# Performance work log

Measured on AMD Instinct MI355X. Metric: run time of the kernel, lower is better.

## Reference

```python
import jax, jax.numpy as jnp
import numpy as np

N_NODES = 100000
N_EDGES = 1200000
D = 64
EPS = 1e-12  # matches torch F.normalize eps


def l2norm(x):
    n = jnp.linalg.norm(x, axis=-1, keepdims=True)
    return x / jnp.maximum(n, EPS)


def sage_layer(x, src, dst, Wl, bl, Wr, scale):
    # mechanism.normalize: row-wise L2 normalize (noise_scale=0 -> perturb is identity)
    xn = l2norm(x)
    # agg = x_normalized + scatter-add of neighbor (source) features into targets
    agg = xn + jax.ops.segment_sum(xn[src], dst, num_segments=N_NODES)
    # MessageNorm(learn_scale=True): normalize(msg) * ||x||_2 * scale
    msg = l2norm(agg) * jnp.linalg.norm(x, axis=-1, keepdims=True) * scale
    # lin_l(msg) + lin_r(x)  (root_weight=True, lin_r has no bias)
    out = msg @ Wl.T + bl + x @ Wr.T
    return l2norm(out)


def setup_inputs() -> dict:
    key = jax.random.key(0)
    ks = jax.random.split(key, 7)
    s = 1.0 / np.sqrt(D)
    return {
        "x": jax.random.normal(ks[0], (N_NODES, D), jnp.float32),
        "Wl0": jax.random.normal(ks[1], (D, D), jnp.float32) * s,
        "bl0": jnp.zeros((D,), jnp.float32),
        "Wr0": jax.random.normal(ks[2], (D, D), jnp.float32) * s,
        "scale0": jnp.ones((), jnp.float32),
        "Wl1": jax.random.normal(ks[3], (D, D), jnp.float32) * s,
        "bl1": jnp.zeros((D,), jnp.float32),
        "Wr1": jax.random.normal(ks[4], (D, D), jnp.float32) * s,
        "scale1": jnp.ones((), jnp.float32),
        "edge_index": jax.random.randint(ks[5], (2, N_EDGES), 0, N_NODES, dtype=jnp.int32),
    }


def reference(x, Wl0, bl0, Wr0, scale0, Wl1, bl1, Wr1, scale1, edge_index):
    src, dst = edge_index[0], edge_index[1]
    h = sage_layer(x, src, dst, Wl0, bl0, Wr0, scale0)
    h = jax.nn.relu(h)  # activation after layer 0 (not pred layer); dropout=identity (eval)
    h = sage_layer(h, src, dst, Wl1, bl1, Wr1, scale1)
    return h  # last layer of pred module: no bn/dropout/activation
```

## Files before the change

kernel.cpp:

```cpp
#include <hip/hip_runtime.h>

#define D 64
#define EPS 1e-12f
#define WPITCH 68
#define BSHIFT 8
#define BW 256
#define NBMAX 2048
#define NBLK 256

typedef unsigned short u16;

__device__ __forceinline__ float bf2f(u16 u) {
    return __uint_as_float(((unsigned)u) << 16);
}
__device__ __forceinline__ u16 f2bf(float f) {
    unsigned u = __float_as_uint(f);
    u += 0x7fffu + ((u >> 16) & 1u);
    return (u16)(u >> 16);
}
__device__ __forceinline__ float loadf(const void* p, size_t i, int bf) {
    return bf ? bf2f(((const u16*)p)[i]) : ((const float*)p)[i];
}
__device__ __forceinline__ float4 cvt4(ushort4 u) {
    return make_float4(bf2f(u.x), bf2f(u.y), bf2f(u.z), bf2f(u.w));
}

#define FMA4(acc, s, v)                       \
    do {                                      \
        acc.x = fmaf((s), (v).x, acc.x);      \
        acc.y = fmaf((s), (v).y, acc.y);      \
        acc.z = fmaf((s), (v).z, acc.z);      \
        acc.w = fmaf((s), (v).w, acc.w);      \
    } while (0)

__global__ __launch_bounds__(64) void detect_kernel(const u16* __restrict__ x,
                                                    int* __restrict__ flag) {
    int lane = threadIdx.x;
    int bad = 0;
    for (int i = 0; i < 64; ++i) {
        u16 u = x[lane * 64 + i];
        int e = (u >> 7) & 0xFF;
        if (e >= 0xC0) bad = 1;
    }
    unsigned long long b = __ballot(bad);
    if (lane == 0) *flag = (b == 0ull) ? 1 : 0;
}


__global__ __launch_bounds__(256) void zero_kernel(int* __restrict__ a, int n) {
    int i = blockIdx.x * blockDim.x + threadIdx.x;
    if (i < n) a[i] = 0;
}

__global__ __launch_bounds__(256) void bhist_kernel(const int* __restrict__ dst,
                                                    int* __restrict__ blockhist,
                                                    int E, int NB) {
    __shared__ int lh[NBMAX];
    const int b = blockIdx.x, t = threadIdx.x;
    const int per = (E + NBLK - 1) / NBLK;
    const int e0 = b * per, e1 = min(E, e0 + per);
    if (NB <= NBMAX) {
        for (int i = t; i < NB; i += 256) lh[i] = 0;
        __syncthreads();
        for (int e = e0 + t; e < e1; e += 256)
            atomicAdd(&lh[dst[e] >> BSHIFT], 1);
        __syncthreads();
        for (int i = t; i < NB; i += 256) blockhist[i * NBLK + b] = lh[i];
    } else {
        for (int e = e0 + t; e < e1; e += 256)
            atomicAdd(&blockhist[(dst[e] >> BSHIFT) * NBLK + b], 1);
    }
}

__global__ __launch_bounds__(256) void scanA_kernel(const int* __restrict__ a,
                                                    int* __restrict__ partials, int M) {
    int b = blockIdx.x, t = threadIdx.x;
    int base = b * 1024 + t * 4;
    int s = 0;
#pragma unroll
    for (int i = 0; i < 4; ++i) {
        int idx = base + i;
        if (idx < M) s += a[idx];
    }
    s += __shfl_xor(s, 32); s += __shfl_xor(s, 16); s += __shfl_xor(s, 8);
    s += __shfl_xor(s, 4);  s += __shfl_xor(s, 2);  s += __shfl_xor(s, 1);
    __shared__ int wt[4];
    if ((t & 63) == 0) wt[t >> 6] = s;
    __syncthreads();
    if (t == 0) partials[b] = wt[0] + wt[1] + wt[2] + wt[3];
}

__global__ __launch_bounds__(64) void scanB_kernel(int* __restrict__ partials, int NP) {
    int l = threadIdx.x;
    int total = 0;
    for (int base = 0; base < NP; base += 64) {
        int v = (base + l < NP) ? partials[base + l] : 0;
        int inc = v;
        for (int d = 1; d < 64; d <<= 1) {
            int u = __shfl_up(inc, d);
            if (l >= d) inc += u;
        }
        if (base + l < NP) partials[base + l] = inc - v + total;
        total += __shfl(inc, 63);
    }
}

__global__ __launch_bounds__(256) void scanC_kernel(const int* __restrict__ a,
                                                    const int* __restrict__ partials,
                                                    int* __restrict__ pos, int M) {
    int b = blockIdx.x, t = threadIdx.x;
    int base = b * 1024 + t * 4;
    int v[4];
    int s = 0;
#pragma unroll
    for (int i = 0; i < 4; ++i) {
        int idx = base + i;
        v[i] = (idx < M) ? a[idx] : 0;
        s += v[i];
    }
    int li = t & 63, w = t >> 6;
    int inc = s;
    for (int d = 1; d < 64; d <<= 1) {
        int u = __shfl_up(inc, d);
        if (li >= d) inc += u;
    }
    __shared__ int wt[4];
    if (li == 63) wt[w] = inc;
    __syncthreads();
    int woff = 0;
    for (int i = 0; i < w; ++i) woff += wt[i];
    int run = partials[b] + woff + (inc - s);
#pragma unroll
    for (int i = 0; i < 4; ++i) {
        int idx = base + i;
        if (idx < M) { pos[idx] = run; run += v[i]; }
    }
}

__global__ __launch_bounds__(256) void bmeta_kernel(const int* __restrict__ pos,
                                                    int* __restrict__ bcounts,
                                                    int* __restrict__ boffsets,
                                                    int NB, int E) {
    int i = blockIdx.x * blockDim.x + threadIdx.x;
    if (i < NB) {
        int s = pos[(size_t)i * NBLK];
        boffsets[i] = s;
        int nxt = (i + 1 < NB) ? pos[(size_t)(i + 1) * NBLK] : E;
        bcounts[i] = nxt - s;
    }
}

__global__ __launch_bounds__(256) void bfill_kernel(const int* __restrict__ src,
                                                    const int* __restrict__ dst,
                                                    int* __restrict__ pos,
                                                    int* __restrict__ bucket,
                                                    int E, int NB) {
    __shared__ int cur[NBMAX];
    const int b = blockIdx.x, t = threadIdx.x;
    const int per = (E + NBLK - 1) / NBLK;
    const int e0 = b * per, e1 = min(E, e0 + per);
    if (NB <= NBMAX) {
        for (int i = t; i < NB; i += 256) cur[i] = pos[(size_t)i * NBLK + b];
        __syncthreads();
        for (int e = e0 + t; e < e1; e += 256) {
            int s = src[e], d = dst[e];
            int p = atomicAdd(&cur[d >> BSHIFT], 1);
            bucket[p] = (s << BSHIFT) | (d & (BW - 1));
        }
    } else {
        for (int e = e0 + t; e < e1; e += 256) {
            int s = src[e], d = dst[e];
            int p = atomicAdd(&pos[(size_t)(d >> BSHIFT) * NBLK + b], 1);
            bucket[p] = (s << BSHIFT) | (d & (BW - 1));
        }
    }
}

__global__ __launch_bounds__(256) void csr_from_buckets_kernel(
    const int* __restrict__ bucket,
    const int* __restrict__ bcounts, const int* __restrict__ boffsets,
    int* __restrict__ counts, int* __restrict__ offsets,
    int* __restrict__ sorted_src, int N)
{
    __shared__ int hist[BW];
    __shared__ int cur[BW];
    __shared__ int wt[4];

    const int b = blockIdx.x;
    const int t = threadIdx.x;
    const int nbase = b << BSHIFT;
    const int ecnt = bcounts[b];
    const int ebase = boffsets[b];

    hist[t] = 0;
    __syncthreads();

    for (int e = t; e < ecnt; e += 256)
        atomicAdd(&hist[bucket[ebase + e] & (BW - 1)], 1);
    __syncthreads();

    int v = hist[t];
    int inc = v;
    for (int d = 1; d < 64; d <<= 1) {
        int u = __shfl_up(inc, d);
        if ((t & 63) >= d) inc += u;
    }
    if ((t & 63) == 63) wt[t >> 6] = inc;
    __syncthreads();
    int woff = 0;
    for (int i = 0; i < (t >> 6); ++i) woff += wt[i];
    int excl = inc - v + woff;
    cur[t] = excl;
    int node = nbase + t;
    if (node < N) {
        counts[node] = v;
        offsets[node] = ebase + excl;
    }
    __syncthreads();

    for (int e = t; e < ecnt; e += 256) {
        int pv = bucket[ebase + e];
        int p = atomicAdd(&cur[pv & (BW - 1)], 1);
        sorted_src[ebase + p] = ((unsigned)pv) >> BSHIFT;
    }
}


__global__ __launch_bounds__(256) void norm_init_kernel(
    const void* __restrict__ xin, float* __restrict__ nx, float* __restrict__ rnx,
    int N, const int* __restrict__ flagp)
{
    const int bf = *flagp;
    int node = (int)((blockIdx.x * blockDim.x + threadIdx.x) >> 6);
    int lane = threadIdx.x & 63;
    if (node >= N) return;
    float v = loadf(xin, (size_t)node * D + lane, bf);
    float s = v * v;
    s += __shfl_xor(s, 32); s += __shfl_xor(s, 16); s += __shfl_xor(s, 8);
    s += __shfl_xor(s, 4);  s += __shfl_xor(s, 2);  s += __shfl_xor(s, 1);
    if (lane == 0) {
        float n = sqrtf(s);
        nx[node] = n;
        rnx[node] = 1.0f / fmaxf(n, EPS);
    }
}

__device__ __forceinline__ float4 loadrow4(const void* p, int row, int lane16, int bf) {
    if (bf) {
        ushort4 u = ((const ushort4*)((const u16*)p + (size_t)row * D))[lane16];
        return cvt4(u);
    }
    return ((const float4*)((const float*)p + (size_t)row * D))[lane16];
}

__global__ __launch_bounds__(256) void gather_kernel(
    const int* __restrict__ offsets, const int* __restrict__ counts,
    const int* __restrict__ sorted_src,
    const void* __restrict__ xin, const float* __restrict__ rnx,
    float* __restrict__ agg, int N, const int* __restrict__ flagp)
{
    const int bf = *flagp;
    int node = (int)((blockIdx.x * blockDim.x + threadIdx.x) >> 6);
    int lane = threadIdx.x & 63;
    if (node >= N) return;
    const int lane16 = lane & 15, grp = lane >> 4;

    float4 acc = make_float4(0.f, 0.f, 0.f, 0.f);
    if (grp == 0) {
        float4 xs = loadrow4(xin, node, lane16, bf);
        FMA4(acc, rnx[node], xs);
    }

    const int start = offsets[node];
    const int deg = counts[node];
    for (int i = 0; i < deg; i += 64) {
        int cnt = min(deg - i, 64);
        int id = (lane < cnt) ? sorted_src[start + i + lane] : 0;
        float wvl = rnx[id];
        int j = 0;
        for (; j + 8 <= cnt; j += 8) {
            int s0 = __shfl(id, j + grp);
            int s1 = __shfl(id, j + 4 + grp);
            float w0 = __shfl(wvl, j + grp);
            float w1 = __shfl(wvl, j + 4 + grp);
            float4 v0 = loadrow4(xin, s0, lane16, bf);
            float4 v1 = loadrow4(xin, s1, lane16, bf);
            FMA4(acc, w0, v0);
            FMA4(acc, w1, v1);
        }
        if (j + 4 <= cnt) {
            int s0 = __shfl(id, j + grp);
            float w0 = __shfl(wvl, j + grp);
            float4 v0 = loadrow4(xin, s0, lane16, bf);
            FMA4(acc, w0, v0);
            j += 4;
        }
        if (j < cnt) {
            int e = j + grp;
            int s0 = __shfl(id, min(e, cnt - 1));
            float w0 = __shfl(wvl, min(e, cnt - 1));
            if (e < cnt) {
                float4 v0 = loadrow4(xin, s0, lane16, bf);
                FMA4(acc, w0, v0);
            }
        }
    }

    acc.x += __shfl_xor(acc.x, 16); acc.y += __shfl_xor(acc.y, 16);
    acc.z += __shfl_xor(acc.z, 16); acc.w += __shfl_xor(acc.w, 16);
    acc.x += __shfl_xor(acc.x, 32); acc.y += __shfl_xor(acc.y, 32);
    acc.z += __shfl_xor(acc.z, 32); acc.w += __shfl_xor(acc.w, 32);
    if (grp == 0)
        ((float4*)(agg + (size_t)node * D))[lane16] = acc;
}

#define KSTEP(kk, comp)                                                     \
    {                                                                       \
        float4 a = *((const float4*)(wlp + (kk) * WPITCH));                 \
        float4 b = *((const float4*)(wrp + (kk) * WPITCH));                 \
        FMA4(acc[0], m[0].comp, a); FMA4(acc[0], xf[0].comp, b);            \
        FMA4(acc[1], m[1].comp, a); FMA4(acc[1], xf[1].comp, b);            \
        FMA4(acc[2], m[2].comp, a); FMA4(acc[2], xf[2].comp, b);            \
        FMA4(acc[3], m[3].comp, a); FMA4(acc[3], xf[3].comp, b);            \
    }

__global__ __launch_bounds__(256) void epilogue_kernel(
    const float* __restrict__ agg, float* __restrict__ nx,
    float* __restrict__ rnx, const void* __restrict__ xin,
    const void* __restrict__ wl, const void* __restrict__ bl,
    const void* __restrict__ wr, const void* __restrict__ scale_p,
    void* __restrict__ out, int N, const int* __restrict__ flagp,
    int relu, int write_norm)
{
    __shared__ float lds_wl[D * WPITCH];
    __shared__ float lds_wr[D * WPITCH];
    __shared__ float lds_bl[D];

    const int bf = *flagp;
    const int t = threadIdx.x;
    for (int idx = t; idx < D * D; idx += 256) {
        int j = idx >> 6, k = idx & 63;
        lds_wl[k * WPITCH + j] = loadf(wl, idx, bf);
        lds_wr[k * WPITCH + j] = loadf(wr, idx, bf);
    }
    if (t < D) lds_bl[t] = loadf(bl, t, bf);
    __syncthreads();

    const float scl = loadf(scale_p, 0, bf);
    const int w = t >> 6, lane = t & 63;
    const int sub = lane >> 4, cg = lane & 15;

    const int node0 = blockIdx.x * 64 + w * 16 + sub * 4;
    int n[4];
    bool valid[4];
    float minv[4];
#pragma unroll
    for (int r = 0; r < 4; ++r) {
        int nn = node0 + r;
        valid[r] = nn < N;
        n[r] = valid[r] ? nn : N - 1;
    }
#pragma unroll
    for (int r = 0; r < 4; ++r) {
        float4 v4 = ((const float4*)(agg + (size_t)n[r] * D))[cg];
        float s = v4.x * v4.x + v4.y * v4.y + v4.z * v4.z + v4.w * v4.w;
        s += __shfl_xor(s, 1); s += __shfl_xor(s, 2);
        s += __shfl_xor(s, 4); s += __shfl_xor(s, 8);
        minv[r] = scl * nx[n[r]] / fmaxf(sqrtf(s), EPS);
    }

    float4 acc[4];
    {
        float4 b4 = ((const float4*)lds_bl)[cg];
#pragma unroll
        for (int r = 0; r < 4; ++r) acc[r] = b4;
    }

    const float* wlbase = lds_wl + cg * 4;
    const float* wrbase = lds_wr + cg * 4;

    if (bf) {
#pragma unroll
        for (int k4 = 0; k4 < 16; ++k4) {
            float4 m[4], xf[4];
#pragma unroll
            for (int r = 0; r < 4; ++r) {
                float4 g4 = ((const float4*)(agg + (size_t)n[r] * D))[k4];
                m[r] = make_float4(g4.x * minv[r], g4.y * minv[r],
                                   g4.z * minv[r], g4.w * minv[r]);
                ushort4 xu = ((const ushort4*)((const u16*)xin + (size_t)n[r] * D))[k4];
                xf[r] = cvt4(xu);
            }
            const float* wlp = wlbase + (k4 * 4) * WPITCH;
            const float* wrp = wrbase + (k4 * 4) * WPITCH;
            KSTEP(0, x) KSTEP(1, y) KSTEP(2, z) KSTEP(3, w)
        }
    } else {
#pragma unroll
        for (int k4 = 0; k4 < 16; ++k4) {
            float4 m[4], xf[4];
#pragma unroll
            for (int r = 0; r < 4; ++r) {
                float4 g4 = ((const float4*)(agg + (size_t)n[r] * D))[k4];
                m[r] = make_float4(g4.x * minv[r], g4.y * minv[r],
                                   g4.z * minv[r], g4.w * minv[r]);
                xf[r] = ((const float4*)((const float*)xin + (size_t)n[r] * D))[k4];
            }
            const float* wlp = wlbase + (k4 * 4) * WPITCH;
            const float* wrp = wrbase + (k4 * 4) * WPITCH;
            KSTEP(0, x) KSTEP(1, y) KSTEP(2, z) KSTEP(3, w)
        }
    }

#pragma unroll
    for (int r = 0; r < 4; ++r) {
        float4 v = acc[r];
        float s2 = v.x * v.x + v.y * v.y + v.z * v.z + v.w * v.w;
        s2 += __shfl_xor(s2, 1); s2 += __shfl_xor(s2, 2);
        s2 += __shfl_xor(s2, 4); s2 += __shfl_xor(s2, 8);
        float inv = 1.0f / fmaxf(sqrtf(s2), EPS);
        float4 rv = make_float4(v.x * inv, v.y * inv, v.z * inv, v.w * inv);
        if (relu) {
            rv.x = fmaxf(rv.x, 0.f); rv.y = fmaxf(rv.y, 0.f);
            rv.z = fmaxf(rv.z, 0.f); rv.w = fmaxf(rv.w, 0.f);
        }
        if (write_norm) {
            float s3 = rv.x * rv.x + rv.y * rv.y + rv.z * rv.z + rv.w * rv.w;
            s3 += __shfl_xor(s3, 1); s3 += __shfl_xor(s3, 2);
            s3 += __shfl_xor(s3, 4); s3 += __shfl_xor(s3, 8);
            if (valid[r] && cg == 0) {
                float nn = sqrtf(s3);
                nx[n[r]] = nn;
                rnx[n[r]] = 1.0f / fmaxf(nn, EPS);
            }
        }
        if (valid[r]) {
            if (bf) {
                ushort4 o = make_ushort4(f2bf(rv.x), f2bf(rv.y), f2bf(rv.z), f2bf(rv.w));
                ((ushort4*)((u16*)out + (size_t)n[r] * D))[cg] = o;
            } else {
                ((float4*)((float*)out + (size_t)n[r] * D))[cg] = rv;
            }
        }
    }
}

extern "C" void kernel_launch(void* const* d_in, const int* in_sizes, int n_in,
                              void* d_out, int out_size, void* d_ws, size_t ws_size,
                              hipStream_t stream)
{
    const void* x   = d_in[0];
    const void* Wl0 = d_in[1];
    const void* bl0 = d_in[2];
    const void* Wr0 = d_in[3];
    const void* sc0 = d_in[4];
    const void* Wl1 = d_in[5];
    const void* bl1 = d_in[6];
    const void* Wr1 = d_in[7];
    const void* sc1 = d_in[8];
    const int* ei   = (const int*)d_in[9];

    const int N = in_sizes[0] / D;
    const int E = in_sizes[9] / 2;
    const int* src = ei;
    const int* dst = ei + E;

    const int NB = (N + BW - 1) >> BSHIFT;
    const int M  = NB * NBLK;
    const int NP = (M + 1023) / 1024;

    float* agg       = (float*)d_ws;
    float* nx        = agg + (size_t)N * D;
    float* rnx       = nx + N;
    int* flag        = (int*)(rnx + N);
    int* counts      = flag + 1;
    int* offsets     = counts + N;
    int* bcounts     = offsets + N;
    int* boffsets    = bcounts + NB;
    int* blockhist   = boffsets + NB;
    int* pos         = blockhist + M;
    int* partials    = pos + M;
    int* bucket      = partials + NP;
    int* sorted_src  = bucket + E;

    void* h = d_out;

    dim3 blk(256);
    int gridA  = (N + 3) / 4;
    int gridC  = (N + 63) / 64;

    detect_kernel<<<1, 64, 0, stream>>>((const u16*)x, flag);

    if (NB > NBMAX)
        zero_kernel<<<(M + 255) / 256, blk, 0, stream>>>(blockhist, M);
    bhist_kernel<<<NBLK, blk, 0, stream>>>(dst, blockhist, E, NB);
    scanA_kernel<<<NP, blk, 0, stream>>>(blockhist, partials, M);
    scanB_kernel<<<1, 64, 0, stream>>>(partials, NP);
    scanC_kernel<<<NP, blk, 0, stream>>>(blockhist, partials, pos, M);
    bmeta_kernel<<<(NB + 255) / 256, blk, 0, stream>>>(pos, bcounts, boffsets, NB, E);
    bfill_kernel<<<NBLK, blk, 0, stream>>>(src, dst, pos, bucket, E, NB);
    csr_from_buckets_kernel<<<NB, blk, 0, stream>>>(bucket, bcounts, boffsets,
                                                    counts, offsets, sorted_src, N);

    norm_init_kernel<<<gridA, blk, 0, stream>>>(x, nx, rnx, N, flag);
    gather_kernel<<<gridA, blk, 0, stream>>>(offsets, counts, sorted_src, x, rnx,
                                             agg, N, flag);
    epilogue_kernel<<<gridC, blk, 0, stream>>>(agg, nx, rnx, x, Wl0, bl0, Wr0, sc0,
                                               h, N, flag, 1, 1);

    gather_kernel<<<gridA, blk, 0, stream>>>(offsets, counts, sorted_src, h, rnx,
                                             agg, N, flag);
    epilogue_kernel<<<gridC, blk, 0, stream>>>(agg, nx, rnx, h, Wl1, bl1, Wr1, sc1,
                                               d_out, N, flag, 0, 0);
}
```

Baseline: 372.4 us.

## Fuse neighbor gather with dense epilogue into a single per-layer kernel

Merges the gather and epilogue kernels into one kernel per layer. Each wavefront now aggregates 16 nodes sequentially and stages the normalized messages in shared memory instead of writing and re-reading a global agg buffer. Norms are double-buffered, and the intermediate layer output moves to workspace so in-place reads and writes do not race. This removes one N×64 float round trip through global memory per layer, plus two launches. In exchange, each block now does a serial 16-node gather per wave with fewer, larger blocks, which could reduce the parallelism available to hide latency.

New measurement: 588.7 us. 1.58x slower.

```diff
diff --git a/kernel.cpp b/kernel.cpp
--- a/kernel.cpp
+++ b/kernel.cpp
@@ -253,67 +253,6 @@
     return ((const float4*)((const float*)p + (size_t)row * D))[lane16];
 }
 
-__global__ __launch_bounds__(256) void gather_kernel(
-    const int* __restrict__ offsets, const int* __restrict__ counts,
-    const int* __restrict__ sorted_src,
-    const void* __restrict__ xin, const float* __restrict__ rnx,
-    float* __restrict__ agg, int N, const int* __restrict__ flagp)
-{
-    const int bf = *flagp;
-    int node = (int)((blockIdx.x * blockDim.x + threadIdx.x) >> 6);
-    int lane = threadIdx.x & 63;
-    if (node >= N) return;
-    const int lane16 = lane & 15, grp = lane >> 4;
-
-    float4 acc = make_float4(0.f, 0.f, 0.f, 0.f);
-    if (grp == 0) {
-        float4 xs = loadrow4(xin, node, lane16, bf);
-        FMA4(acc, rnx[node], xs);
-    }
-
-    const int start = offsets[node];
-    const int deg = counts[node];
-    for (int i = 0; i < deg; i += 64) {
-        int cnt = min(deg - i, 64);
-        int id = (lane < cnt) ? sorted_src[start + i + lane] : 0;
-        float wvl = rnx[id];
-        int j = 0;
-        for (; j + 8 <= cnt; j += 8) {
-            int s0 = __shfl(id, j + grp);
-            int s1 = __shfl(id, j + 4 + grp);
-            float w0 = __shfl(wvl, j + grp);
-            float w1 = __shfl(wvl, j + 4 + grp);
-            float4 v0 = loadrow4(xin, s0, lane16, bf);
-            float4 v1 = loadrow4(xin, s1, lane16, bf);
-            FMA4(acc, w0, v0);
-            FMA4(acc, w1, v1);
-        }
-        if (j + 4 <= cnt) {
-            int s0 = __shfl(id, j + grp);
-            float w0 = __shfl(wvl, j + grp);
-            float4 v0 = loadrow4(xin, s0, lane16, bf);
-            FMA4(acc, w0, v0);
-            j += 4;
-        }
-        if (j < cnt) {
-            int e = j + grp;
-            int s0 = __shfl(id, min(e, cnt - 1));
-            float w0 = __shfl(wvl, min(e, cnt - 1));
-            if (e < cnt) {
-                float4 v0 = loadrow4(xin, s0, lane16, bf);
-                FMA4(acc, w0, v0);
-            }
-        }
-    }
-
-    acc.x += __shfl_xor(acc.x, 16); acc.y += __shfl_xor(acc.y, 16);
-    acc.z += __shfl_xor(acc.z, 16); acc.w += __shfl_xor(acc.w, 16);
-    acc.x += __shfl_xor(acc.x, 32); acc.y += __shfl_xor(acc.y, 32);
-    acc.z += __shfl_xor(acc.z, 32); acc.w += __shfl_xor(acc.w, 32);
-    if (grp == 0)
-        ((float4*)(agg + (size_t)node * D))[lane16] = acc;
-}
-
 #define KSTEP(kk, comp)                                                     \
     {                                                                       \
         float4 a = *((const float4*)(wlp + (kk) * WPITCH));                 \
@@ -324,9 +263,12 @@
         FMA4(acc[3], m[3].comp, a); FMA4(acc[3], xf[3].comp, b);            \
     }
 
-__global__ __launch_bounds__(256) void epilogue_kernel(
-    const float* __restrict__ agg, float* __restrict__ nx,
-    float* __restrict__ rnx, const void* __restrict__ xin,
+__global__ __launch_bounds__(256) void fused_layer_kernel(
+    const int* __restrict__ offsets, const int* __restrict__ counts,
+    const int* __restrict__ sorted_src,
+    const void* __restrict__ xin,
+    const float* __restrict__ nx_in, const float* __restrict__ rnx_in,
+    float* __restrict__ nx_out, float* __restrict__ rnx_out,
     const void* __restrict__ wl, const void* __restrict__ bl,
     const void* __restrict__ wr, const void* __restrict__ scale_p,
     void* __restrict__ out, int N, const int* __restrict__ flagp,
@@ -335,6 +277,7 @@
     __shared__ float lds_wl[D * WPITCH];
     __shared__ float lds_wr[D * WPITCH];
     __shared__ float lds_bl[D];
+    __shared__ float msgbuf[4][16 * WPITCH];
 
     const int bf = *flagp;
     const int t = threadIdx.x;
@@ -349,25 +292,81 @@
     const float scl = loadf(scale_p, 0, bf);
     const int w = t >> 6, lane = t & 63;
     const int sub = lane >> 4, cg = lane & 15;
-
-    const int node0 = blockIdx.x * 64 + w * 16 + sub * 4;
+    const int lane16 = cg, grp = sub;
+    float* mrow = msgbuf[w];
+
+    const int nodebase = blockIdx.x * 64 + w * 16;
+
+    for (int g = 0; g < 16; ++g) {
+        int node = nodebase + g;
+        int nc = (node < N) ? node : N - 1;
+
+        float4 acc = make_float4(0.f, 0.f, 0.f, 0.f);
+        if (grp == 0) {
+            float4 xs = loadrow4(xin, nc, lane16, bf);
+            FMA4(acc, rnx_in[nc], xs);
+        }
+
+        const int start = offsets[nc];
+        const int deg = counts[nc];
+        for (int i = 0; i < deg; i += 64) {
+            int cnt = min(deg - i, 64);
+            int id = (lane < cnt) ? sorted_src[start + i + lane] : 0;
+            float wvl = rnx_in[id];
+            int j = 0;
+            for (; j + 8 <= cnt; j += 8) {
+                int s0 = __shfl(id, j + grp);
+                int s1 = __shfl(id, j + 4 + grp);
+                float w0 = __shfl(wvl, j + grp);
+                float w1 = __shfl(wvl, j + 4 + grp);
+                float4 v0 = loadrow4(xin, s0, lane16, bf);
+                float4 v1 = loadrow4(xin, s1, lane16, bf);
+                FMA4(acc, w0, v0);
+                FMA4(acc, w1, v1);
+            }
+            if (j + 4 <= cnt) {
+                int s0 = __shfl(id, j + grp);
+                float w0 = __shfl(wvl, j + grp);
+                float4 v0 = loadrow4(xin, s0, lane16, bf);
+                FMA4(acc, w0, v0);
+                j += 4;
+            }
+            if (j < cnt) {
+                int e = j + grp;
+                int s0 = __shfl(id, min(e, cnt - 1));
+                float w0 = __shfl(wvl, min(e, cnt - 1));
+                if (e < cnt) {
+                    float4 v0 = loadrow4(xin, s0, lane16, bf);
+                    FMA4(acc, w0, v0);
+                }
+            }
+        }
+
+        acc.x += __shfl_xor(acc.x, 16); acc.y += __shfl_xor(acc.y, 16);
+        acc.z += __shfl_xor(acc.z, 16); acc.w += __shfl_xor(acc.w, 16);
+        acc.x += __shfl_xor(acc.x, 32); acc.y += __shfl_xor(acc.y, 32);
+        acc.z += __shfl_xor(acc.z, 32); acc.w += __shfl_xor(acc.w, 32);
+
+        float s = acc.x * acc.x + acc.y * acc.y + acc.z * acc.z + acc.w * acc.w;
+        s += __shfl_xor(s, 1); s += __shfl_xor(s, 2);
+        s += __shfl_xor(s, 4); s += __shfl_xor(s, 8);
+        float mv = scl * nx_in[nc] / fmaxf(sqrtf(s), EPS);
+
+        if (grp == 0) {
+            *((float4*)(mrow + g * WPITCH + lane16 * 4)) =
+                make_float4(acc.x * mv, acc.y * mv, acc.z * mv, acc.w * mv);
+        }
+    }
+
+    const int node0 = nodebase + sub * 4;
     int n[4];
     bool valid[4];
-    float minv[4];
 #pragma unroll
     for (int r = 0; r < 4; ++r) {
         int nn = node0 + r;
         valid[r] = nn < N;
         n[r] = valid[r] ? nn : N - 1;
     }
-#pragma unroll
-    for (int r = 0; r < 4; ++r) {
-        float4 v4 = ((const float4*)(agg + (size_t)n[r] * D))[cg];
-        float s = v4.x * v4.x + v4.y * v4.y + v4.z * v4.z + v4.w * v4.w;
-        s += __shfl_xor(s, 1); s += __shfl_xor(s, 2);
-        s += __shfl_xor(s, 4); s += __shfl_xor(s, 8);
-        minv[r] = scl * nx[n[r]] / fmaxf(sqrtf(s), EPS);
-    }
 
     float4 acc[4];
     {
@@ -385,9 +384,7 @@
             float4 m[4], xf[4];
 #pragma unroll
             for (int r = 0; r < 4; ++r) {
-                float4 g4 = ((const float4*)(agg + (size_t)n[r] * D))[k4];
-                m[r] = make_float4(g4.x * minv[r], g4.y * minv[r],
-                                   g4.z * minv[r], g4.w * minv[r]);
+                m[r] = *((const float4*)(mrow + (sub * 4 + r) * WPITCH + k4 * 4));
                 ushort4 xu = ((const ushort4*)((const u16*)xin + (size_t)n[r] * D))[k4];
                 xf[r] = cvt4(xu);
             }
@@ -401,9 +398,7 @@
             float4 m[4], xf[4];
 #pragma unroll
             for (int r = 0; r < 4; ++r) {
-                float4 g4 = ((const float4*)(agg + (size_t)n[r] * D))[k4];
-                m[r] = make_float4(g4.x * minv[r], g4.y * minv[r],
-                                   g4.z * minv[r], g4.w * minv[r]);
+                m[r] = *((const float4*)(mrow + (sub * 4 + r) * WPITCH + k4 * 4));
                 xf[r] = ((const float4*)((const float*)xin + (size_t)n[r] * D))[k4];
             }
             const float* wlp = wlbase + (k4 * 4) * WPITCH;
@@ -430,8 +425,8 @@
             s3 += __shfl_xor(s3, 4); s3 += __shfl_xor(s3, 8);
             if (valid[r] && cg == 0) {
                 float nn = sqrtf(s3);
-                nx[n[r]] = nn;
-                rnx[n[r]] = 1.0f / fmaxf(nn, EPS);
+                nx_out[n[r]] = nn;
+                rnx_out[n[r]] = 1.0f / fmaxf(nn, EPS);
             }
         }
         if (valid[r]) {
@@ -469,10 +464,12 @@
     const int M  = NB * NBLK;
     const int NP = (M + 1023) / 1024;
 
-    float* agg       = (float*)d_ws;
-    float* nx        = agg + (size_t)N * D;
+    float* hbuf      = (float*)d_ws;
+    float* nx        = hbuf + (size_t)N * D;
     float* rnx       = nx + N;
-    int* flag        = (int*)(rnx + N);
+    float* nx2       = rnx + N;
+    float* rnx2      = nx2 + N;
+    int* flag        = (int*)(rnx2 + N);
     int* counts      = flag + 1;
     int* offsets     = counts + N;
     int* bcounts     = offsets + N;
@@ -483,7 +480,7 @@
     int* bucket      = partials + NP;
     int* sorted_src  = bucket + E;
 
-    void* h = d_out;
+    void* h = hbuf;
 
     dim3 blk(256);
     int gridA  = (N + 3) / 4;
@@ -503,13 +500,11 @@
                                                     counts, offsets, sorted_src, N);
 
     norm_init_kernel<<<gridA, blk, 0, stream>>>(x, nx, rnx, N, flag);
-    gather_kernel<<<gridA, blk, 0, stream>>>(offsets, counts, sorted_src, x, rnx,
-                                             agg, N, flag);
-    epilogue_kernel<<<gridC, blk, 0, stream>>>(agg, nx, rnx, x, Wl0, bl0, Wr0, sc0,
-                                               h, N, flag, 1, 1);
-
-    gather_kernel<<<gridA, blk, 0, stream>>>(offsets, counts, sorted_src, h, rnx,
-                                             agg, N, flag);
-    epilogue_kernel<<<gridC, blk, 0, stream>>>(agg, nx, rnx, h, Wl1, bl1, Wr1, sc1,
-                                               d_out, N, flag, 0, 0);
-}
+    fused_layer_kernel<<<gridC, blk, 0, stream>>>(
+        offsets, counts, sorted_src, x, nx, rnx, nx2, rnx2,
+        Wl0, bl0, Wr0, sc0, h, N, flag, 1, 1);
+
+    fused_layer_kernel<<<gridC, blk, 0, stream>>>(
+        offsets, counts, sorted_src, h, nx2, rnx2, nx, rnx,
+        Wl1, bl1, Wr1, sc1, d_out, N, flag, 0, 0);
+}
```
